# Performance work log

Measured on AMD Instinct MI355X. Metric: run time of the kernel, lower is better.

## Reference

```python
import jax, jax.numpy as jnp
import numpy as np
from jax import lax

VOCAB = 32000
D = 256      # d_model
N = 16       # n_neurons
NL = 6       # n_layers
DS = 16      # d_state
DC = 4       # d_conv
DI = 512     # d_inner = expand * d_model
DTR = 16     # dt_rank = ceil(D/16)
NH = 4       # attention heads
HD = D // NH
B, L = 1, 128


def setup_inputs() -> dict:
    key = jax.random.key(0)
    ks = list(jax.random.split(key, 32))
    it = iter(ks)

    def rn(shape, scale):
        return jax.random.normal(next(it), shape, jnp.float32) * scale

    p = {}
    p["x"] = jax.random.randint(next(it), (B, L), 0, VOCAB, dtype=jnp.int32)
    p["embedding"] = rn((VOCAB, D), 0.02)
    p["norm1_w"] = jnp.ones((NL, D)); p["norm1_b"] = jnp.zeros((NL, D))
    p["norm2_w"] = jnp.ones((NL, D)); p["norm2_b"] = jnp.zeros((NL, D))
    # Mamba params (stacked over layers)
    p["in_proj_w"] = rn((NL, 2 * DI, D), D ** -0.5)
    p["conv_w"] = rn((NL, DI, DC), DC ** -0.5)
    p["conv_b"] = jnp.zeros((NL, DI))
    p["x_proj_w"] = rn((NL, DTR + 2 * DS, DI), DI ** -0.5)
    p["dt_proj_w"] = rn((NL, DI, DTR), DTR ** -0.5)
    dt0 = jax.random.uniform(next(it), (NL, DI), jnp.float32, 1e-3, 1e-1)
    p["dt_proj_b"] = jnp.log(jnp.expm1(dt0))  # inverse softplus init
    p["A_log"] = jnp.log(jnp.tile(jnp.arange(1.0, DS + 1.0, dtype=jnp.float32), (NL, DI, 1)))
    p["skip_D"] = jnp.ones((NL, DI))
    p["out_proj_w"] = rn((NL, D, DI), DI ** -0.5)
    # cross-neuron MHA params
    p["attn_in_w"] = rn((NL, 3 * D, D), D ** -0.5)
    p["attn_in_b"] = jnp.zeros((NL, 3 * D))
    p["attn_out_w"] = rn((NL, D, D), D ** -0.5)
    p["attn_out_b"] = jnp.zeros((NL, D))
    p["norm_f_w"] = jnp.ones((D,)); p["norm_f_b"] = jnp.zeros((D,))
    p["head_b"] = jnp.zeros((VOCAB,))
    return p


def _ln(x, w, b):
    m = x.mean(-1, keepdims=True)
    v = ((x - m) ** 2).mean(-1, keepdims=True)
    return (x - m) * lax.rsqrt(v + 1e-5) * w + b


def _mamba(x, ipw, cw, cb, xpw, dpw, dpb, alog, dskip, opw):
    # x: (BN, L, D)
    BN, Ls, _ = x.shape
    xz = x @ ipw.T                       # (BN, L, 2*DI)
    u, z = xz[..., :DI], xz[..., DI:]
    # depthwise causal conv1d, kernel DC, left-pad DC-1
    uc = lax.conv_general_dilated(
        u.swapaxes(1, 2), cw[:, None, :], (1,), [(DC - 1, 0)],
        dimension_numbers=("NCH", "OIH", "NCH"), feature_group_count=DI)
    u = jax.nn.silu(uc + cb[None, :, None]).swapaxes(1, 2)  # (BN, L, DI)
    xdbl = u @ xpw.T                     # (BN, L, DTR+2*DS)
    dt = jax.nn.softplus(xdbl[..., :DTR] @ dpw.T + dpb)     # (BN, L, DI)
    Bm = xdbl[..., DTR:DTR + DS]
    Cm = xdbl[..., DTR + DS:]
    A = -jnp.exp(alog)                   # (DI, DS)

    def step(h, ins):
        dt_t, b_t, c_t, u_t = ins        # (BN,DI) (BN,DS) (BN,DS) (BN,DI)
        h = jnp.exp(dt_t[..., None] * A) * h + (dt_t * u_t)[..., None] * b_t[:, None, :]
        return h, jnp.einsum("bds,bs->bd", h, c_t)

    h0 = jnp.zeros((BN, DI, DS), x.dtype)
    _, ys = lax.scan(step, h0, (dt.swapaxes(0, 1), Bm.swapaxes(0, 1),
                                Cm.swapaxes(0, 1), u.swapaxes(0, 1)))
    y = ys.swapaxes(0, 1) + u * dskip
    return (y * jax.nn.silu(z)) @ opw.T


def _mha(x, iw, ib, ow, ob):
    # x: (B*L, N, D); self-attention across neurons
    Bq, S, _ = x.shape
    qkv = x @ iw.T + ib
    q, k, v = jnp.split(qkv, 3, axis=-1)
    q = q.reshape(Bq, S, NH, HD); k = k.reshape(Bq, S, NH, HD); v = v.reshape(Bq, S, NH, HD)
    att = jax.nn.softmax(jnp.einsum("bqhd,bkhd->bhqk", q, k) / np.float32(np.sqrt(HD)), axis=-1)
    o = jnp.einsum("bhqk,bkhd->bqhd", att, v).reshape(Bq, S, D)
    return o @ ow.T + ob


def reference(x, embedding, norm1_w, norm1_b, norm2_w, norm2_b, in_proj_w, conv_w,
              conv_b, x_proj_w, dt_proj_w, dt_proj_b, A_log, skip_D, out_proj_w,
              attn_in_w, attn_in_b, attn_out_w, attn_out_b, norm_f_w, norm_f_b, head_b):
    Bb, Ll = x.shape
    h = embedding[x]                                             # (B, L, D)
    h = jnp.broadcast_to(h[:, None], (Bb, N, Ll, D)).reshape(Bb * N, Ll, D)
    for i in range(NL):
        h = h + _mamba(_ln(h, norm1_w[i], norm1_b[i]), in_proj_w[i], conv_w[i],
                       conv_b[i], x_proj_w[i], dt_proj_w[i], dt_proj_b[i],
                       A_log[i], skip_D[i], out_proj_w[i])
        xc = _ln(h, norm2_w[i], norm2_b[i]).reshape(Bb, N, Ll, D)
        xc = xc.transpose(0, 2, 1, 3).reshape(Bb * Ll, N, D)
        co = _mha(xc, attn_in_w[i], attn_in_b[i], attn_out_w[i], attn_out_b[i])
        h = h + co.reshape(Bb, Ll, N, D).transpose(0, 2, 1, 3).reshape(Bb * N, Ll, D)
    h = h.reshape(Bb, N, Ll, D).mean(axis=1)                     # avg over neurons
    return _ln(h, norm_f_w, norm_f_b) @ embedding.T + head_b     # tied head
```

## Files before the change

kernel.cpp:

```cpp
#include <hip/hip_runtime.h>

constexpr int SEQ    = 128;
constexpr int NVOCAB = 32000;

constexpr size_t O_HA = 0;
constexpr size_t O_HB = O_HA + (size_t)SEQ*256;
constexpr size_t O_U  = O_HB + (size_t)SEQ*256;
constexpr size_t O_DT = O_U  + (size_t)SEQ*512;
constexpr size_t O_ZS = O_DT + (size_t)SEQ*512;
constexpr size_t O_BC = O_ZS + (size_t)SEQ*512;
constexpr size_t O_YG = O_BC + (size_t)SEQ*32;
constexpr size_t O_AH = O_YG + (size_t)SEQ*512;

__device__ __forceinline__ float wsum(float p) {
    #pragma unroll
    for (int m = 1; m < 64; m <<= 1) p += __shfl_xor(p, m);
    return p;
}
__device__ __forceinline__ float dot4(float4 a, float4 b) {
    return a.x*b.x + a.y*b.y + a.z*b.z + a.w*b.w;
}

template<int MR, int KK>
__device__ __forceinline__ void gemmX(
    const float* __restrict__ Wg, const float* __restrict__ A, int AS,
    float* __restrict__ dest, int DS,
    const float* __restrict__ addsrc, int ASS, const float* __restrict__ bias)
{
    const int lane = threadIdx.x & 63;
    const int wv   = threadIdx.x >> 6;
    const int tq = lane & 3, cs = lane >> 2;
    const int c  = wv*16 + cs;
    const float* Wp = Wg + (size_t)c*KK + tq*8;
    float acc[MR];
    #pragma unroll
    for (int r = 0; r < MR; ++r) acc[r] = 0.0f;

    float4 w0a = *(const float4*)(Wp);
    float4 w0b = *(const float4*)(Wp + 4);
    float4 w1a, w1b;
    #pragma unroll
    for (int kc = 0; kc < KK; kc += 64) {
        if (kc + 32 < KK) {
            w1a = *(const float4*)(Wp + kc + 32);
            w1b = *(const float4*)(Wp + kc + 36);
        }
        #pragma unroll
        for (int r = 0; r < MR; ++r) {
            float4 a0 = *(const float4*)&A[r*AS + kc + tq*8];
            float4 a1 = *(const float4*)&A[r*AS + kc + tq*8 + 4];
            acc[r] += dot4(a0, w0a) + dot4(a1, w0b);
        }
        if (kc + 64 < KK) {
            w0a = *(const float4*)(Wp + kc + 64);
            w0b = *(const float4*)(Wp + kc + 68);
        }
        if (kc + 32 < KK) {
            #pragma unroll
            for (int r = 0; r < MR; ++r) {
                float4 a0 = *(const float4*)&A[r*AS + kc + 32 + tq*8];
                float4 a1 = *(const float4*)&A[r*AS + kc + 36 + tq*8];
                acc[r] += dot4(a0, w1a) + dot4(a1, w1b);
            }
        }
    }
    #pragma unroll
    for (int r = 0; r < MR; ++r) {
        float v = acc[r];
        v += __shfl_xor(v, 1);
        v += __shfl_xor(v, 2);
        acc[r] = v;
    }
    if (tq == 0) {
        #pragma unroll
        for (int r = 0; r < MR; ++r) {
            float v = acc[r];
            if (bias)   v += bias[c];
            if (addsrc) v += addsrc[r*ASS + c];
            dest[r*DS + c] = v;
        }
    }
}

__device__ __forceinline__ void ln_row(const float* __restrict__ src, float* __restrict__ dst,
                                       const float* __restrict__ w, const float* __restrict__ b)
{
    int lane = threadIdx.x & 63;
    float4 x = *(const float4*)&src[lane*4];
    float sm = wsum(x.x + x.y + x.z + x.w);
    float mean = sm * (1.0f/256.0f);
    float d0 = x.x-mean, d1 = x.y-mean, d2 = x.z-mean, d3 = x.w-mean;
    float var = wsum(d0*d0 + d1*d1 + d2*d2 + d3*d3) * (1.0f/256.0f);
    float rstd = rsqrtf(var + 1e-5f);
    float4 ww = *(const float4*)&w[lane*4];
    float4 bb = *(const float4*)&b[lane*4];
    float4 o;
    o.x = d0*rstd*ww.x + bb.x;
    o.y = d1*rstd*ww.y + bb.y;
    o.z = d2*rstd*ww.z + bb.z;
    o.w = d3*rstd*ww.w + bb.w;
    *(float4*)&dst[lane*4] = o;
}

__global__ __launch_bounds__(1024) void rowk_kernel(
    const int* __restrict__ x, const float* __restrict__ emb,
    const float* __restrict__ n1w_l, const float* __restrict__ n1b_l,
    const float* __restrict__ n2w_l, const float* __restrict__ n2b_l,
    const float* __restrict__ ipw_l, const float* __restrict__ cw_l, const float* __restrict__ cb_l,
    const float* __restrict__ xpw_l, const float* __restrict__ dpw_l, const float* __restrict__ dpb_l,
    const float* __restrict__ opw_l, const float* __restrict__ aivw_l, const float* __restrict__ aivb_l,
    const float* __restrict__ aow_l, const float* __restrict__ aob_l,
    const float* __restrict__ nfw, const float* __restrict__ nfb,
    const float* __restrict__ hin, float* __restrict__ hout,
    const float* __restrict__ ygv, float* __restrict__ uv, float* __restrict__ dtv,
    float* __restrict__ zsv, float* __restrict__ bcv, float* __restrict__ AH,
    int li)
{
    __shared__ float SM[6336];
    float* hP  = SM;
    float* h1  = SM + 1056;
    float* sLN = SM + 2112;
    float* sAX = SM + 3168;
    float* zR  = SM + 5248;
    float* suR = SM + 5760;
    float* sxR = SM + 6272;

    const int r = blockIdx.x;
    const int tid = threadIdx.x;
    const int lane = tid & 63, wv = tid >> 6;
    int rr[4];
    #pragma unroll
    for (int j = 0; j < 4; ++j) { int v = r - 3 + j; rr[j] = v < 0 ? 0 : v; }

    {
        int hr = tid >> 8, hc = tid & 255;
        if (li <= 1) hP[hr*264 + hc] = emb[(size_t)x[rr[hr]]*256 + hc];
        else         hP[hr*264 + hc] = hin[rr[hr]*256 + hc];
    }
    __syncthreads();

    float* hC = hP;
    if (li >= 1) {
        {
            int yr = tid >> 9, yc = tid & 511;
            sAX[yr*520 + yc]     = ygv[rr[yr]*512 + yc];
            sAX[(2+yr)*520 + yc] = ygv[rr[2+yr]*512 + yc];
        }
        __syncthreads();
        gemmX<4,512>(opw_l, sAX, 520, h1, 264, hP, 264, nullptr);
        __syncthreads();
        if (wv < 4) ln_row(h1 + wv*264, sLN + wv*264, n2w_l, n2b_l);
        __syncthreads();
        gemmX<4,256>(aivw_l, sLN, 264, sAX, 520, nullptr, 0, aivb_l);
        __syncthreads();
        gemmX<4,256>(aow_l, sAX, 520, h1, 264, h1, 264, aob_l);
        __syncthreads();
        hC = h1;
        if (tid < 256) hout[r*256 + tid] = h1[3*264 + tid];
        if (li == 6) {
            if (tid < 256) {
                float v = h1[3*264 + tid];
                float s = wsum(v);
                float q = wsum(v*v);
                if (lane == 0) { sxR[wv] = s; sxR[8 + wv] = q; }
            }
            __syncthreads();
            if (tid < 256) {
                float v = h1[3*264 + tid];
                float mean = (sxR[0]+sxR[1]+sxR[2]+sxR[3]) * (1.0f/256.0f);
                float var  = (sxR[8]+sxR[9]+sxR[10]+sxR[11]) * (1.0f/256.0f) - mean*mean;
                float rstd = rsqrtf(var + 1e-5f);
                AH[r*256 + tid] = (v - mean)*rstd*nfw[tid] + nfb[tid];
            }
            return;
        }
    }

    if (wv < 4) ln_row(hC + wv*264, sLN + wv*264, n1w_l, n1b_l);
    __syncthreads();
    gemmX<4,256>(ipw_l,                   sLN, 264, sAX,       520, nullptr, 0, nullptr);
    __syncthreads();
    gemmX<4,256>(ipw_l + (size_t)256*256, sLN, 264, sAX + 256, 520, nullptr, 0, nullptr);
    __syncthreads();
    gemmX<1,256>(ipw_l + (size_t)512*256, sLN + 3*264, 264, zR,       512, nullptr, 0, nullptr);
    __syncthreads();
    gemmX<1,256>(ipw_l + (size_t)768*256, sLN + 3*264, 264, zR + 256, 512, nullptr, 0, nullptr);
    __syncthreads();

    if (tid < 512) {
        int d = tid;
        float4 c4 = *(const float4*)&cw_l[d*4];
        float acc = cb_l[d];
        if (r >= 3) acc += sAX[d]        * c4.x;
        if (r >= 2) acc += sAX[520 + d]  * c4.y;
        if (r >= 1) acc += sAX[1040 + d] * c4.z;
        acc += sAX[1560 + d] * c4.w;
        float sg = acc / (1.0f + __expf(-acc));
        suR[d] = sg;
        uv[r*512 + d] = sg;
        float z = zR[d];
        zsv[r*512 + d] = z / (1.0f + __expf(-z));
    }
    __syncthreads();

    {
        float4 a0 = *(const float4*)&suR[lane*4];
        float4 a1 = *(const float4*)&suR[256 + lane*4];
        float p[3];
        #pragma unroll
        for (int j = 0; j < 3; ++j) {
            int c = wv*3 + j;
            float4 q0 = *(const float4*)&xpw_l[(size_t)c*512 + lane*4];
            float4 q1 = *(const float4*)&xpw_l[(size_t)c*512 + 256 + lane*4];
            p[j] = dot4(a0, q0) + dot4(a1, q1);
        }
        #pragma unroll
        for (int m = 1; m < 64; m <<= 1) {
            #pragma unroll
            for (int j = 0; j < 3; ++j) p[j] += __shfl_xor(p[j], m);
        }
        if (lane == 0) {
            #pragma unroll
            for (int j = 0; j < 3; ++j) sxR[wv*3 + j] = p[j];
        }
    }
    __syncthreads();
    if (tid >= 16 && tid < 48) bcv[r*32 + tid - 16] = sxR[tid];

    if (tid < 512) {
        int d = tid;
        float4 sx0 = *(const float4*)&sxR[0];
        float4 sx1 = *(const float4*)&sxR[4];
        float4 sx2 = *(const float4*)&sxR[8];
        float4 sx3 = *(const float4*)&sxR[12];
        const float4* dp = (const float4*)&dpw_l[(size_t)d*16];
        float acc = dpb_l[d] + dot4(dp[0], sx0) + dot4(dp[1], sx1)
                             + dot4(dp[2], sx2) + dot4(dp[3], sx3);
        dtv[r*512 + d] = fmaxf(acc, 0.0f) + log1pf(__expf(-fabsf(acc)));
    }
}

__global__ __launch_bounds__(256) void scan_kernel(
    const float* __restrict__ dt, const float* __restrict__ u, const float* __restrict__ zs,
    const float* __restrict__ bcv,
    const float* __restrict__ alog_l, const float* __restrict__ dsk_l,
    float* __restrict__ yg)
{
    __shared__ float s5[5*128];
    float* sdt = s5;        float* su2 = s5 + 128;
    float* sz2 = s5 + 256;  float* sB  = s5 + 384;  float* sC = s5 + 512;
    int tid = threadIdx.x;
    int s  = tid & 15, dl = tid >> 4;
    int d0 = blockIdx.x * 16;
    int d  = d0 + dl;
    float a_ds = -__expf(alog_l[d*16 + s]);
    float dskv = dsk_l[d];
    float hst = 0.0f;
    for (int t0 = 0; t0 < SEQ; t0 += 8) {
        __syncthreads();
        if (tid < 128) {
            int tt = tid >> 4, j = tid & 15;
            int t = t0 + tt;
            sdt[tt*16+j] = dt[t*512 + d0 + j];
            su2[tt*16+j] = u [t*512 + d0 + j];
            sz2[tt*16+j] = zs[t*512 + d0 + j];
        } else {
            int q = tid - 128;
            int tt = q >> 4, j = q & 15;
            int t = t0 + tt;
            sB[tt*16+j] = bcv[t*32 + j];
            sC[tt*16+j] = bcv[t*32 + 16 + j];
        }
        __syncthreads();
        #pragma unroll
        for (int tt = 0; tt < 8; ++tt) {
            float dtvv = sdt[tt*16+dl];
            float uvv  = su2[tt*16+dl];
            hst = __expf(dtvv * a_ds) * hst + dtvv * uvv * sB[tt*16+s];
            float p = hst * sC[tt*16+s];
            p += __shfl_xor(p, 1);
            p += __shfl_xor(p, 2);
            p += __shfl_xor(p, 4);
            p += __shfl_xor(p, 8);
            if (s == 0) {
                float y = p + uvv * dskv;
                yg[(t0+tt)*512 + d] = y * sz2[tt*16+dl];
            }
        }
    }
}

__global__ __launch_bounds__(256) void head_kernel(
    const float* __restrict__ AH, const float* __restrict__ emb,
    const float* __restrict__ hb, float* __restrict__ out)
{
    __shared__ float sA[32*129];
    __shared__ float sW[32*129];
    int tid = threadIdx.x;
    int c0 = blockIdx.x * 128;
    int rr = tid >> 1;
    int kj = (tid & 1) * 16;
    int r4 = (tid >> 4) * 4;
    int c4 = (tid & 15) * 4;
    float acc[8][8] = {};

    for (int kc = 0; kc < 256; kc += 32) {
        __syncthreads();
        #pragma unroll
        for (int i = 0; i < 4; ++i) {
            float4 a = *(const float4*)&AH[(size_t)rr*256 + kc + kj + i*4];
            sA[(kj+i*4+0)*129 + rr] = a.x;
            sA[(kj+i*4+1)*129 + rr] = a.y;
            sA[(kj+i*4+2)*129 + rr] = a.z;
            sA[(kj+i*4+3)*129 + rr] = a.w;
            float4 w = *(const float4*)&emb[(size_t)(c0+rr)*256 + kc + kj + i*4];
            sW[(kj+i*4+0)*129 + rr] = w.x;
            sW[(kj+i*4+1)*129 + rr] = w.y;
            sW[(kj+i*4+2)*129 + rr] = w.z;
            sW[(kj+i*4+3)*129 + rr] = w.w;
        }
        __syncthreads();
        #pragma unroll
        for (int k = 0; k < 32; ++k) {
            float4 a0 = *(const float4*)&sA[k*129 + r4];
            float4 a1 = *(const float4*)&sA[k*129 + 64 + r4];
            float4 b0 = *(const float4*)&sW[k*129 + c4];
            float4 b1 = *(const float4*)&sW[k*129 + 64 + c4];
            float av[8] = {a0.x,a0.y,a0.z,a0.w, a1.x,a1.y,a1.z,a1.w};
            float bv[8] = {b0.x,b0.y,b0.z,b0.w, b1.x,b1.y,b1.z,b1.w};
            #pragma unroll
            for (int i = 0; i < 8; ++i)
                #pragma unroll
                for (int j = 0; j < 8; ++j)
                    acc[i][j] += av[i]*bv[j];
        }
    }
    #pragma unroll
    for (int i = 0; i < 8; ++i) {
        int r = (i < 4) ? (r4 + i) : (64 + r4 + i - 4);
        #pragma unroll
        for (int jh = 0; jh < 2; ++jh) {
            int c = c0 + jh*64 + c4;
            float4 h4 = *(const float4*)&hb[c];
            float4 o;
            o.x = acc[i][jh*4+0] + h4.x;
            o.y = acc[i][jh*4+1] + h4.y;
            o.z = acc[i][jh*4+2] + h4.z;
            o.w = acc[i][jh*4+3] + h4.w;
            *(float4*)&out[(size_t)r*NVOCAB + c] = o;
        }
    }
}

extern "C" void kernel_launch(void* const* d_in, const int* in_sizes, int n_in,
                              void* d_out, int out_size, void* d_ws, size_t ws_size,
                              hipStream_t stream)
{
    const int*   xin = (const int*)d_in[0];
    const float* emb = (const float*)d_in[1];
    const float* n1w = (const float*)d_in[2];
    const float* n1b = (const float*)d_in[3];
    const float* n2w = (const float*)d_in[4];
    const float* n2b = (const float*)d_in[5];
    const float* ipw = (const float*)d_in[6];
    const float* cw  = (const float*)d_in[7];
    const float* cb  = (const float*)d_in[8];
    const float* xpw = (const float*)d_in[9];
    const float* dpw = (const float*)d_in[10];
    const float* dpb = (const float*)d_in[11];
    const float* alog= (const float*)d_in[12];
    const float* dsk = (const float*)d_in[13];
    const float* opw = (const float*)d_in[14];
    const float* aiw = (const float*)d_in[15];
    const float* aib = (const float*)d_in[16];
    const float* aow = (const float*)d_in[17];
    const float* aob = (const float*)d_in[18];
    const float* nfw = (const float*)d_in[19];
    const float* nfb = (const float*)d_in[20];
    const float* hb  = (const float*)d_in[21];
    float* ws  = (float*)d_ws;
    float* out = (float*)d_out;

    for (int i = 0; i <= 6; ++i) {
        int ka = i <= 5 ? i : 5;
        int kc = i >= 1 ? i - 1 : 0;
        const float* hin  = (i % 2 == 0) ? ws + O_HA : ws + O_HB;
        float*       hout = (i % 2 == 0) ? ws + O_HB : ws + O_HA;
        rowk_kernel<<<128, 1024, 0, stream>>>(
            xin, emb,
            n1w + ka*256, n1b + ka*256,
            n2w + kc*256, n2b + kc*256,
            ipw + (size_t)ka*1024*256, cw + (size_t)ka*512*4, cb + ka*512,
            xpw + (size_t)ka*48*512, dpw + (size_t)ka*512*16, dpb + ka*512,
            opw + (size_t)kc*256*512,
            aiw + (size_t)kc*768*256 + (size_t)512*256, aib + kc*768 + 512,
            aow + (size_t)kc*256*256, aob + kc*256,
            nfw, nfb,
            hin, hout,
            ws + O_YG, ws + O_U, ws + O_DT, ws + O_ZS, ws + O_BC, ws + O_AH,
            i);
        if (i <= 5)
            scan_kernel<<<32, 256, 0, stream>>>(
                ws + O_DT, ws + O_U, ws + O_ZS, ws + O_BC,
                alog + (size_t)i*512*16, dsk + i*512, ws + O_YG);
    }
    head_kernel<<<NVOCAB/128, 256, 0, stream>>>(ws + O_AH, emb, hb, out);
}
```

Baseline: 588.4 us.

## Preload full scan inputs once and retile head GEMM with register prefetch

```diff
diff --git a/kernel.cpp b/kernel.cpp
--- a/kernel.cpp
+++ b/kernel.cpp
@@ -240,53 +240,71 @@
     }
 }
 
-__global__ __launch_bounds__(256) void scan_kernel(
+__global__ __launch_bounds__(128) void scan_kernel(
     const float* __restrict__ dt, const float* __restrict__ u, const float* __restrict__ zs,
     const float* __restrict__ bcv,
     const float* __restrict__ alog_l, const float* __restrict__ dsk_l,
     float* __restrict__ yg)
 {
-    __shared__ float s5[5*128];
-    float* sdt = s5;        float* su2 = s5 + 128;
-    float* sz2 = s5 + 256;  float* sB  = s5 + 384;  float* sC = s5 + 512;
-    int tid = threadIdx.x;
-    int s  = tid & 15, dl = tid >> 4;
-    int d0 = blockIdx.x * 16;
-    int d  = d0 + dl;
-    float a_ds = -__expf(alog_l[d*16 + s]);
-    float dskv = dsk_l[d];
+    __shared__ float sdt[8*132];
+    __shared__ float su2[8*132];
+    __shared__ float sz2[8*132];
+    __shared__ float sB [16*132];
+    __shared__ float sC [16*132];
+    const int tid = threadIdx.x;
+    const int s  = tid & 15;
+    const int dl = tid >> 4;
+    const int d0 = blockIdx.x * 8;
+    const int d  = d0 + dl;
+
+    {
+        const int t = tid;
+        float4 q0, q1;
+        q0 = *(const float4*)&dt[t*512 + d0];
+        q1 = *(const float4*)&dt[t*512 + d0 + 4];
+        sdt[0*132+t]=q0.x; sdt[1*132+t]=q0.y; sdt[2*132+t]=q0.z; sdt[3*132+t]=q0.w;
+        sdt[4*132+t]=q1.x; sdt[5*132+t]=q1.y; sdt[6*132+t]=q1.z; sdt[7*132+t]=q1.w;
+        q0 = *(const float4*)&u[t*512 + d0];
+        q1 = *(const float4*)&u[t*512 + d0 + 4];
+        su2[0*132+t]=q0.x; su2[1*132+t]=q0.y; su2[2*132+t]=q0.z; su2[3*132+t]=q0.w;
+        su2[4*132+t]=q1.x; su2[5*132+t]=q1.y; su2[6*132+t]=q1.z; su2[7*132+t]=q1.w;
+        q0 = *(const float4*)&zs[t*512 + d0];
+        q1 = *(const float4*)&zs[t*512 + d0 + 4];
+        sz2[0*132+t]=q0.x; sz2[1*132+t]=q0.y; sz2[2*132+t]=q0.z; sz2[3*132+t]=q0.w;
+        sz2[4*132+t]=q1.x; sz2[5*132+t]=q1.y; sz2[6*132+t]=q1.z; sz2[7*132+t]=q1.w;
+        float4 b0 = *(const float4*)&bcv[t*32 + 0];
+        float4 b1 = *(const float4*)&bcv[t*32 + 4];
+        float4 b2 = *(const float4*)&bcv[t*32 + 8];
+        float4 b3 = *(const float4*)&bcv[t*32 + 12];
+        sB[ 0*132+t]=b0.x; sB[ 1*132+t]=b0.y; sB[ 2*132+t]=b0.z; sB[ 3*132+t]=b0.w;
+        sB[ 4*132+t]=b1.x; sB[ 5*132+t]=b1.y; sB[ 6*132+t]=b1.z; sB[ 7*132+t]=b1.w;
+        sB[ 8*132+t]=b2.x; sB[ 9*132+t]=b2.y; sB[10*132+t]=b2.z; sB[11*132+t]=b2.w;
+        sB[12*132+t]=b3.x; sB[13*132+t]=b3.y; sB[14*132+t]=b3.z; sB[15*132+t]=b3.w;
+        float4 c0 = *(const float4*)&bcv[t*32 + 16];
+        float4 c1 = *(const float4*)&bcv[t*32 + 20];
+        float4 c2 = *(const float4*)&bcv[t*32 + 24];
+        float4 c3 = *(const float4*)&bcv[t*32 + 28];
+        sC[ 0*132+t]=c0.x; sC[ 1*132+t]=c0.y; sC[ 2*132+t]=c0.z; sC[ 3*132+t]=c0.w;
+        sC[ 4*132+t]=c1.x; sC[ 5*132+t]=c1.y; sC[ 6*132+t]=c1.z; sC[ 7*132+t]=c1.w;
+        sC[ 8*132+t]=c2.x; sC[ 9*132+t]=c2.y; sC[10*132+t]=c2.z; sC[11*132+t]=c2.w;
+        sC[12*132+t]=c3.x; sC[13*132+t]=c3.y; sC[14*132+t]=c3.z; sC[15*132+t]=c3.w;
+    }
+    __syncthreads();
+
+    const float a_ds = -__expf(alog_l[d*16 + s]);
+    const float dskv = dsk_l[d];
     float hst = 0.0f;
-    for (int t0 = 0; t0 < SEQ; t0 += 8) {
-        __syncthreads();
-        if (tid < 128) {
-            int tt = tid >> 4, j = tid & 15;
-            int t = t0 + tt;
-            sdt[tt*16+j] = dt[t*512 + d0 + j];
-            su2[tt*16+j] = u [t*512 + d0 + j];
-            sz2[tt*16+j] = zs[t*512 + d0 + j];
-        } else {
-            int q = tid - 128;
-            int tt = q >> 4, j = q & 15;
-            int t = t0 + tt;
-            sB[tt*16+j] = bcv[t*32 + j];
-            sC[tt*16+j] = bcv[t*32 + 16 + j];
-        }
-        __syncthreads();
-        #pragma unroll
-        for (int tt = 0; tt < 8; ++tt) {
-            float dtvv = sdt[tt*16+dl];
-            float uvv  = su2[tt*16+dl];
-            hst = __expf(dtvv * a_ds) * hst + dtvv * uvv * sB[tt*16+s];
-            float p = hst * sC[tt*16+s];
-            p += __shfl_xor(p, 1);
-            p += __shfl_xor(p, 2);
-            p += __shfl_xor(p, 4);
-            p += __shfl_xor(p, 8);
-            if (s == 0) {
-                float y = p + uvv * dskv;
-                yg[(t0+tt)*512 + d] = y * sz2[tt*16+dl];
-            }
-        }
+    #pragma unroll 8
+    for (int t = 0; t < SEQ; ++t) {
+        float dtvv = sdt[dl*132 + t];
+        float uvv  = su2[dl*132 + t];
+        hst = __expf(dtvv * a_ds) * hst + dtvv * uvv * sB[s*132 + t];
+        float p = hst * sC[s*132 + t];
+        p += __shfl_xor(p, 1);
+        p += __shfl_xor(p, 2);
+        p += __shfl_xor(p, 4);
+        p += __shfl_xor(p, 8);
+        if (s == 0) yg[t*512 + d] = (p + uvv * dskv) * sz2[dl*132 + t];
     }
 }
 
@@ -294,61 +312,73 @@
     const float* __restrict__ AH, const float* __restrict__ emb,
     const float* __restrict__ hb, float* __restrict__ out)
 {
-    __shared__ float sA[32*129];
-    __shared__ float sW[32*129];
-    int tid = threadIdx.x;
-    int c0 = blockIdx.x * 128;
-    int rr = tid >> 1;
-    int kj = (tid & 1) * 16;
-    int r4 = (tid >> 4) * 4;
-    int c4 = (tid & 15) * 4;
-    float acc[8][8] = {};
+    __shared__ float sA[32*132];
+    __shared__ float sW[32*68];
+    const int tid = threadIdx.x;
+    const int c0  = blockIdx.x * 64;
+    const int ar = tid >> 1;
+    const int ak = (tid & 1) * 16;
+    const int wc = tid & 63;
+    const int wk = (tid >> 6) * 8;
+    const int rg = tid >> 4;
+    const int cg = tid & 15;
+
+    const float* Ap = AH  + (size_t)ar*256 + ak;
+    const float* Wp = emb + (size_t)(c0 + wc)*256 + wk;
+
+    float4 ra0 = *(const float4*)(Ap + 0);
+    float4 ra1 = *(const float4*)(Ap + 4);
+    float4 ra2 = *(const float4*)(Ap + 8);
+    float4 ra3 = *(const float4*)(Ap + 12);
+    float4 rw0 = *(const float4*)(Wp + 0);
+    float4 rw1 = *(const float4*)(Wp + 4);
+
+    float acc[8][4] = {};
 
     for (int kc = 0; kc < 256; kc += 32) {
-        __syncthreads();
-        #pragma unroll
-        for (int i = 0; i < 4; ++i) {
-            float4 a = *(const float4*)&AH[(size_t)rr*256 + kc + kj + i*4];
-            sA[(kj+i*4+0)*129 + rr] = a.x;
-            sA[(kj+i*4+1)*129 + rr] = a.y;
-            sA[(kj+i*4+2)*129 + rr] = a.z;
-            sA[(kj+i*4+3)*129 + rr] = a.w;
-            float4 w = *(const float4*)&emb[(size_t)(c0+rr)*256 + kc + kj + i*4];
-            sW[(kj+i*4+0)*129 + rr] = w.x;
-            sW[(kj+i*4+1)*129 + rr] = w.y;
-            sW[(kj+i*4+2)*129 + rr] = w.z;
-            sW[(kj+i*4+3)*129 + rr] = w.w;
-        }
-        __syncthreads();
+        if (kc) __syncthreads();
+        sA[(ak+ 0)*132+ar]=ra0.x; sA[(ak+ 1)*132+ar]=ra0.y; sA[(ak+ 2)*132+ar]=ra0.z; sA[(ak+ 3)*132+ar]=ra0.w;
+        sA[(ak+ 4)*132+ar]=ra1.x; sA[(ak+ 5)*132+ar]=ra1.y; sA[(ak+ 6)*132+ar]=ra1.z; sA[(ak+ 7)*132+ar]=ra1.w;
+        sA[(ak+ 8)*132+ar]=ra2.x; sA[(ak+ 9)*132+ar]=ra2.y; sA[(ak+10)*132+ar]=ra2.z; sA[(ak+11)*132+ar]=ra2.w;
+        sA[(ak+12)*132+ar]=ra3.x; sA[(ak+13)*132+ar]=ra3.y; sA[(ak+14)*132+ar]=ra3.z; sA[(ak+15)*132+ar]=ra3.w;
+        sW[(wk+0)*68+wc]=rw0.x; sW[(wk+1)*68+wc]=rw0.y; sW[(wk+2)*68+wc]=rw0.z; sW[(wk+3)*68+wc]=rw0.w;
+        sW[(wk+4)*68+wc]=rw1.x; sW[(wk+5)*68+wc]=rw1.y; sW[(wk+6)*68+wc]=rw1.z; sW[(wk+7)*68+wc]=rw1.w;
+        __syncthreads();
+        if (kc + 32 < 256) {
+            ra0 = *(const float4*)(Ap + kc + 32);
+            ra1 = *(const float4*)(Ap + kc + 36);
+            ra2 = *(const float4*)(Ap + kc + 40);
+            ra3 = *(const float4*)(Ap + kc + 44);
+            rw0 = *(const float4*)(Wp + kc + 32);
+            rw1 = *(const float4*)(Wp + kc + 36);
+        }
         #pragma unroll
         for (int k = 0; k < 32; ++k) {
-            float4 a0 = *(const float4*)&sA[k*129 + r4];
-            float4 a1 = *(const float4*)&sA[k*129 + 64 + r4];
-            float4 b0 = *(const float4*)&sW[k*129 + c4];
-            float4 b1 = *(const float4*)&sW[k*129 + 64 + c4];
+            float4 a0 = *(const float4*)&sA[k*132 + rg*8];
+            float4 a1 = *(const float4*)&sA[k*132 + rg*8 + 4];
+            float4 b  = *(const float4*)&sW[k*68  + cg*4];
             float av[8] = {a0.x,a0.y,a0.z,a0.w, a1.x,a1.y,a1.z,a1.w};
-            float bv[8] = {b0.x,b0.y,b0.z,b0.w, b1.x,b1.y,b1.z,b1.w};
             #pragma unroll
-            for (int i = 0; i < 8; ++i)
-                #pragma unroll
-                for (int j = 0; j < 8; ++j)
-                    acc[i][j] += av[i]*bv[j];
-        }
-    }
+            for (int i = 0; i < 8; ++i) {
+                acc[i][0] += av[i]*b.x;
+                acc[i][1] += av[i]*b.y;
+                acc[i][2] += av[i]*b.z;
+                acc[i][3] += av[i]*b.w;
+            }
+        }
+    }
+
+    const int c = c0 + cg*4;
+    float4 h4 = *(const float4*)&hb[c];
     #pragma unroll
     for (int i = 0; i < 8; ++i) {
-        int r = (i < 4) ? (r4 + i) : (64 + r4 + i - 4);
-        #pragma unroll
-        for (int jh = 0; jh < 2; ++jh) {
-            int c = c0 + jh*64 + c4;
-            float4 h4 = *(const float4*)&hb[c];
-            float4 o;
-            o.x = acc[i][jh*4+0] + h4.x;
-            o.y = acc[i][jh*4+1] + h4.y;
-            o.z = acc[i][jh*4+2] + h4.z;
-            o.w = acc[i][jh*4+3] + h4.w;
-            *(float4*)&out[(size_t)r*NVOCAB + c] = o;
-        }
+        int r = rg*8 + i;
+        float4 o;
+        o.x = acc[i][0] + h4.x;
+        o.y = acc[i][1] + h4.y;
+        o.z = acc[i][2] + h4.z;
+        o.w = acc[i][3] + h4.w;
+        *(float4*)&out[(size_t)r*NVOCAB + c] = o;
     }
 }
 
@@ -400,9 +430,9 @@
             ws + O_YG, ws + O_U, ws + O_DT, ws + O_ZS, ws + O_BC, ws + O_AH,
             i);
         if (i <= 5)
-            scan_kernel<<<32, 256, 0, stream>>>(
+            scan_kernel<<<64, 128, 0, stream>>>(
                 ws + O_DT, ws + O_U, ws + O_ZS, ws + O_BC,
                 alog + (size_t)i*512*16, dsk + i*512, ws + O_YG);
     }
-    head_kernel<<<NVOCAB/128, 256, 0, stream>>>(ws + O_AH, emb, hb, out);
-}
+    head_kernel<<<NVOCAB/64, 256, 0, stream>>>(ws + O_AH, emb, hb, out);
+}
```

Result: faster. 538.5 us (-8.5%).
